# Performance work log

Measured on AMD Instinct MI355X. Metric: run time of the kernel, lower is better.

Reference implementation:

```python
import jax, jax.numpy as jnp
import numpy as np

T, B, I, H, NL = 512, 64, 1024, 1024, 2  # time, batch, input, hidden, layers


def setup_inputs() -> dict:
    key = jax.random.key(0)
    k0, k1, k2, k3, k4 = jax.random.split(key, 5)
    # xavier-uniform bound for W: [fan_in, 3*H]
    bound = float(np.sqrt(6.0 / (I + 3 * H)))
    x = jax.random.normal(k0, (T, B, I), jnp.float32)
    h0 = jax.random.normal(k1, (NL, B, H), jnp.float32) * 0.1  # initial hidden states
    W1 = jax.random.uniform(k2, (I, 3 * H), jnp.float32, -bound, bound)
    b1 = jnp.zeros((3 * H,), jnp.float32)
    W2 = jax.random.uniform(k3, (H, 3 * H), jnp.float32, -bound, bound)
    b2 = jnp.zeros((3 * H,), jnp.float32)
    L = jax.random.randint(k4, (B,), 0, T)  # per-example valid lengths
    return {"x": x, "h0": h0, "W1": W1, "b1": b1, "W2": W2, "b2": b2, "L": L}


def _lrn_layer(xs, h_init, W, b, L):
    # Hoist the input projection out of the time loop: same math as per-step mm.
    gates = jnp.einsum('tbi,ig->tbg', xs, W) + b          # [T, B, 3H]
    p, q, r = jnp.split(gates, 3, axis=-1)                 # each [T, B, H]
    # mask[t, b] = 1 if t < L[b] else 0 (keeps old state past sequence end)
    mask = (jnp.arange(xs.shape[0])[:, None] < L[None, :]).astype(xs.dtype)[:, :, None]

    def step(h, inp):
        pt, qt, rt, mt = inp
        i = jax.nn.sigmoid(pt + h)
        f = jax.nn.sigmoid(qt - h)
        nh = jnp.tanh(i * rt + f * h)
        nh = nh * mt + h * (1.0 - mt)
        return nh, nh

    h_last, out = jax.lax.scan(step, h_init, (p, q, r, mask))
    return out, h_last


def reference(x, h0, W1, b1, W2, b2, L):
    out1, h1 = _lrn_layer(x, h0[0], W1, b1, L)
    out2, h2 = _lrn_layer(out1, h0[1], W2, b2, L)   # dropout=0 -> identity between layers
    return out2, jnp.stack([h1, h2], axis=0)
```

## Files before the change

### kernel.cpp

```cpp
#include <hip/hip_runtime.h>

#define T_DIM 512
#define B_DIM 64
#define I_DIM 1024
#define H_DIM 1024
#define G3    3072
#define M_DIM (T_DIM * B_DIM)
#define K_DIM 1024
#define KT    16

typedef unsigned short u16;
typedef __bf16 bf16x8 __attribute__((ext_vector_type(8)));
typedef float  f32x4  __attribute__((ext_vector_type(4)));
typedef unsigned short u16x8 __attribute__((ext_vector_type(8)));

__device__ __forceinline__ u16 f2bf(float x) {
  union { float f; unsigned u; } v; v.f = x;
  unsigned r = v.u + 0x7fffu + ((v.u >> 16) & 1u);
  return (u16)(r >> 16);
}
__device__ __forceinline__ float bf2f(u16 x) {
  union { unsigned u; float f; } v; v.u = ((unsigned)x) << 16;
  return v.f;
}

__global__ void build_offsets_kernel(const int* __restrict__ L, int* __restrict__ meta) {
  __shared__ int cnt[T_DIM];
  __shared__ int Ls[B_DIM];
  const int t = threadIdx.x;
  if (t < B_DIM) Ls[t] = L[t];
  __syncthreads();
  int n = 0;
  #pragma unroll 8
  for (int b = 0; b < B_DIM; ++b) n += (Ls[b] > t) ? 1 : 0;
  cnt[t] = n;
  __syncthreads();
  if (t == 0) {
    int acc = 0;
    for (int s = 0; s < T_DIM; ++s) { int c = cnt[s]; cnt[s] = acc; acc += c; }
    meta[T_DIM] = acc;
    meta[513] = acc;
    meta[514] = (acc + 511) & ~511;
  }
  __syncthreads();
  meta[t] = cnt[t];
}

__global__ void build_crow_kernel(const int* __restrict__ L, const int* __restrict__ meta,
                                  int* __restrict__ crow) {
  const int t = blockIdx.x;
  const int b = threadIdx.x;
  const bool valid = t < L[b];
  unsigned long long mask = __ballot(valid);
  const int rank = __popcll(mask & ((1ull << b) - 1ull));
  if (valid) crow[(t << 6) + b] = meta[t] + rank;
}

__global__ void cast_gather_kernel(const float* __restrict__ in, const int* __restrict__ L,
                                   const int* __restrict__ crow, u16* __restrict__ out, int n8) {
  int idx = blockIdx.x * blockDim.x + threadIdx.x;
  int stride = gridDim.x * blockDim.x;
  for (int i = idx; i < n8; i += stride) {
    const int row = i >> 7;
    const int ch  = i & 127;
    const int b = row & 63, t = row >> 6;
    if (t >= L[b]) continue;
    const int cr = crow[row];
    const float4* p = (const float4*)(in + (size_t)row * 1024 + ch * 8);
    float4 a = p[0], bb = p[1];
    u16x8 o;
    o[0] = f2bf(a.x);  o[1] = f2bf(a.y);  o[2] = f2bf(a.z);  o[3] = f2bf(a.w);
    o[4] = f2bf(bb.x); o[5] = f2bf(bb.y); o[6] = f2bf(bb.z); o[7] = f2bf(bb.w);
    *(u16x8*)(out + (size_t)cr * 1024 + ch * 8) = o;
  }
}

__global__ void transpose_cast_kernel(const float* __restrict__ W,
                                      u16* __restrict__ Wt, int K, int N) {
  __shared__ float tile[32][33];
  int n0 = blockIdx.x * 32, k0 = blockIdx.y * 32;
  int tx = threadIdx.x, ty = threadIdx.y;
  #pragma unroll
  for (int dy = 0; dy < 32; dy += 8)
    tile[ty + dy][tx] = W[(size_t)(k0 + ty + dy) * N + n0 + tx];
  __syncthreads();
  #pragma unroll
  for (int dy = 0; dy < 32; dy += 8)
    Wt[(size_t)(n0 + ty + dy) * K + k0 + tx] = f2bf(tile[tx][ty + dy]);
}

__device__ __forceinline__ void gload_lds16(const void* g, void* l) {
  __builtin_amdgcn_global_load_lds(
      (const __attribute__((address_space(1))) void*)g,
      (__attribute__((address_space(3))) void*)l, 16, 0, 0);
}

__device__ __forceinline__ void stage_half(const u16* __restrict__ G, u16* lbuf,
                                           int rb, int k0, int w, int l) {
  const int cs   = (l & 7) ^ (l >> 3);
  const int rsub = l >> 3;
  #pragma unroll
  for (int r = 0; r < 2; ++r) {
    const int row0 = rb + r * 64 + w * 8;
    gload_lds16(G + (size_t)(row0 + rsub) * K_DIM + k0 + cs * 8,
                lbuf + (size_t)row0 * 64);
  }
}

__device__ __forceinline__ bf16x8 ldfrag(const u16* buf, int row, int ks, int fr, int g4) {
  const int slot = ((ks << 2) + g4) ^ (fr & 7);
  return *(const bf16x8*)(buf + (size_t)row * 64 + slot * 8);
}

__device__ __forceinline__ void read_a(const u16* buf, bf16x8 (&dst)[4][2],
                                       int rbase, int fr, int g4) {
  #pragma unroll
  for (int m = 0; m < 4; ++m) {
    dst[m][0] = ldfrag(buf, rbase + m * 16 + fr, 0, fr, g4);
    dst[m][1] = ldfrag(buf, rbase + m * 16 + fr, 1, fr, g4);
  }
}
__device__ __forceinline__ void read_b(const u16* buf, bf16x8 (&dst)[2][2],
                                       int rbase, int fr, int g4) {
  #pragma unroll
  for (int n = 0; n < 2; ++n) {
    dst[n][0] = ldfrag(buf, rbase + n * 16 + fr, 0, fr, g4);
    dst[n][1] = ldfrag(buf, rbase + n * 16 + fr, 1, fr, g4);
  }
}

#define BARRIER()  do { __builtin_amdgcn_s_barrier(); __builtin_amdgcn_sched_barrier(0); } while (0)
#define LGKM0()    do { asm volatile("s_waitcnt lgkmcnt(0)" ::: "memory"); __builtin_amdgcn_sched_barrier(0); } while (0)

#define MFMA_Q(ACC, AV, BV)                                                            \
  do {                                                                                 \
    __builtin_amdgcn_s_setprio(1);                                                     \
    _Pragma("unroll")                                                                  \
    for (int m = 0; m < 4; ++m)                                                        \
      _Pragma("unroll")                                                                \
      for (int n = 0; n < 2; ++n) {                                                    \
        ACC = __builtin_amdgcn_mfma_f32_16x16x32_bf16(AV[m][0], BV[n][0], ACC, 0, 0, 0); \
        ACC = __builtin_amdgcn_mfma_f32_16x16x32_bf16(AV[m][1], BV[n][1], ACC, 0, 0, 0); \
      }                                                                                \
    __builtin_amdgcn_s_setprio(0);                                                     \
  } while (0)

__global__ __launch_bounds__(512, 2) void gemm256_kernel(
    const u16* __restrict__ A, const u16* __restrict__ Bt,
    const float* __restrict__ bias, u16* __restrict__ C, int N,
    const int* __restrict__ meta) {
  __shared__ u16 As[2][256 * 64];
  __shared__ u16 Bs[2][256 * 64];
  const int tid = threadIdx.x;
  const int l  = tid & 63, w = tid >> 6;
  const int wm = w >> 2,  wn = w & 3;
  const int fr = l & 15,  g4 = l >> 4;

  const int ny   = meta[514] >> 8;
  const int nact = gridDim.x * ny;
  const int q    = nact >> 3;
  const int lin  = blockIdx.y * gridDim.x + blockIdx.x;
  const int idx  = lin >> 3;
  if (idx >= q) return;
  const int swz = (lin & 7) * q + idx;
  const int bx = swz % gridDim.x, by = swz / gridDim.x;
  const int bm = by * 256, bn = bx * 256;

  const u16* Ab = A  + (size_t)bm * K_DIM;
  const u16* Bb = Bt + (size_t)bn * K_DIM;

  stage_half(Ab, As[0], 0,   0,  w, l);
  stage_half(Ab, As[0], 128, 0,  w, l);
  stage_half(Bb, Bs[0], 0,   0,  w, l);
  stage_half(Bb, Bs[0], 128, 0,  w, l);
  stage_half(Ab, As[1], 0,   64, w, l);
  stage_half(Ab, As[1], 128, 64, w, l);
  stage_half(Bb, Bs[1], 0,   64, w, l);

  f32x4 acc[8][4] = {};
  bf16x8 av0[4][2], av1[4][2], bv0[2][2], bv1[2][2];

  for (int T = 0; T < KT - 1; ++T) {
    const u16* Ac = As[T & 1];
    const u16* Bc = Bs[T & 1];
    u16* Bn1 = Bs[(T + 1) & 1];
    u16* An2 = As[T & 1];        u16* Bn2 = Bs[T & 1];
    const int k1 = (T + 1) * 64, k2 = (T + 2) * 64;
    const bool st2 = (T + 2) < KT;

    asm volatile("s_waitcnt vmcnt(6)" ::: "memory");
    BARRIER();

    read_a(Ac, av0, wm * 128, fr, g4);
    read_b(Bc, bv0, wn * 64, fr, g4);
    stage_half(Bb, Bn1, 128, k1, w, l);
    LGKM0();

    MFMA_Q(acc[m][n], av0, bv0);
    read_b(Bc, bv1, wn * 64 + 32, fr, g4);
    LGKM0();

    MFMA_Q(acc[m][n + 2], av0, bv1);
    read_a(Ac, av1, wm * 128 + 64, fr, g4);
    LGKM0();
    BARRIER();

    if (st2) {
      stage_half(Ab, An2, 0,   k2, w, l);
      stage_half(Ab, An2, 128, k2, w, l);
      stage_half(Bb, Bn2, 0,   k2, w, l);
    }

    MFMA_Q(acc[m + 4][n + 2], av1, bv1);
    MFMA_Q(acc[m + 4][n],     av1, bv0);
  }

  {
    const u16* Ac = As[(KT - 1) & 1];
    const u16* Bc = Bs[(KT - 1) & 1];
    asm volatile("s_waitcnt vmcnt(0)" ::: "memory");
    BARRIER();
    #pragma unroll
    for (int m = 0; m < 4; ++m) {
      av0[m][0] = ldfrag(Ac, wm * 128 + m * 16 + fr, 0, fr, g4);
      av0[m][1] = ldfrag(Ac, wm * 128 + m * 16 + fr, 1, fr, g4);
      av1[m][0] = ldfrag(Ac, wm * 128 + (m + 4) * 16 + fr, 0, fr, g4);
      av1[m][1] = ldfrag(Ac, wm * 128 + (m + 4) * 16 + fr, 1, fr, g4);
    }
    #pragma unroll
    for (int n = 0; n < 2; ++n) {
      bv0[n][0] = ldfrag(Bc, wn * 64 + n * 16 + fr, 0, fr, g4);
      bv0[n][1] = ldfrag(Bc, wn * 64 + n * 16 + fr, 1, fr, g4);
      bv1[n][0] = ldfrag(Bc, wn * 64 + (n + 2) * 16 + fr, 0, fr, g4);
      bv1[n][1] = ldfrag(Bc, wn * 64 + (n + 2) * 16 + fr, 1, fr, g4);
    }
    LGKM0();
    MFMA_Q(acc[m][n],         av0, bv0);
    MFMA_Q(acc[m][n + 2],     av0, bv1);
    MFMA_Q(acc[m + 4][n + 2], av1, bv1);
    MFMA_Q(acc[m + 4][n],     av1, bv0);
    BARRIER();
  }

  float bb[4];
  #pragma unroll
  for (int j = 0; j < 4; ++j) bb[j] = bias[bn + wn * 64 + j * 16 + fr];

  u16* eb = (w < 4) ? ((u16*)As + (size_t)w * 8192)
                    : ((u16*)Bs + (size_t)(w - 4) * 8192);
  #pragma unroll
  for (int i = 0; i < 8; ++i)
    #pragma unroll
    for (int j = 0; j < 4; ++j)
      #pragma unroll
      for (int v = 0; v < 4; ++v) {
        const int row = i * 16 + g4 * 4 + v;
        const int col = j * 16 + fr;
        eb[row * 64 + (col ^ ((row & 12) << 2))] = f2bf(acc[i][j][v] + bb[j]);
      }
  LGKM0();
  #pragma unroll
  for (int c = 0; c < 16; ++c) {
    const int lrow = c * 8 + (l >> 3);
    const int lcol = (l & 7) * 8;
    u16x8 d = *(const u16x8*)&eb[lrow * 64 + (lcol ^ ((lrow & 12) << 2))];
    *(u16x8*)&C[(size_t)(bm + wm * 128 + lrow) * N + (bn + wn * 64 + lcol)] = d;
  }
}

template <int OUT_BF16>
__global__ void scan_kernel(const u16* __restrict__ gates,
                            const float* __restrict__ h0,
                            const int* __restrict__ L,
                            const int* __restrict__ crow,
                            u16* __restrict__ out_bf,
                            float* __restrict__ out_f,
                            float* __restrict__ hlast) {
  const int e = blockIdx.x * blockDim.x + threadIdx.x;
  const int b = e >> 10;
  const int j = e & 1023;
  float h = h0[e];
  const int Lb = L[b];
  const size_t o0 = (size_t)b * H_DIM + j;
  int t = 0;
  #pragma unroll 8
  for (; t < Lb; ++t) {
    const int cr = crow[(t << 6) + b];
    const size_t gt = (size_t)cr * G3 + j;
    float p = bf2f(gates[gt]);
    float q = bf2f(gates[gt + H_DIM]);
    float r = bf2f(gates[gt + 2 * H_DIM]);
    float ii = 1.f / (1.f + __expf(-(p + h)));
    float ff = 1.f / (1.f + __expf(-(q - h)));
    float u  = ii * r + ff * h;
    float e2 = __expf(2.f * u);
    h = 1.f - 2.f / (e2 + 1.f);
    if (OUT_BF16) out_bf[(size_t)cr * H_DIM + j] = f2bf(h);
    else          out_f [o0 + (size_t)t * (B_DIM * H_DIM)] = h;
  }
  if (!OUT_BF16) {
    for (; t < T_DIM; ++t)
      out_f[o0 + (size_t)t * (B_DIM * H_DIM)] = h;
  }
  hlast[o0] = h;
}

extern "C" void kernel_launch(void* const* d_in, const int* in_sizes, int n_in,
                              void* d_out, int out_size, void* d_ws, size_t ws_size,
                              hipStream_t stream) {
  const float* x  = (const float*)d_in[0];
  const float* h0 = (const float*)d_in[1];
  const float* W1 = (const float*)d_in[2];
  const float* b1 = (const float*)d_in[3];
  const float* W2 = (const float*)d_in[4];
  const float* b2 = (const float*)d_in[5];
  const int*   L  = (const int*)d_in[6];

  float* out2 = (float*)d_out;
  float* hl   = out2 + (size_t)T_DIM * B_DIM * H_DIM;

  char* w = (char*)d_ws;
  u16* xb    = (u16*)(w);
  u16* W1t   = (u16*)(w + (size_t)67108864);
  u16* W2t   = (u16*)(w + (size_t)73400320);
  u16* gates = (u16*)(w + (size_t)79691776);
  u16* out1  = (u16*)(w + (size_t)281018368);
  int* meta  = (int*)(w + (size_t)348127232);
  int* crow  = (int*)(w + (size_t)348131328);

  build_offsets_kernel<<<1, 512, 0, stream>>>(L, meta);
  build_crow_kernel<<<T_DIM, 64, 0, stream>>>(L, meta, crow);
  cast_gather_kernel<<<2048, 256, 0, stream>>>(x, L, crow, xb, (T_DIM * B_DIM * I_DIM) / 8);
  dim3 tb(32, 8);
  transpose_cast_kernel<<<dim3(G3 / 32, I_DIM / 32), tb, 0, stream>>>(W1, W1t, I_DIM, G3);
  transpose_cast_kernel<<<dim3(G3 / 32, H_DIM / 32), tb, 0, stream>>>(W2, W2t, H_DIM, G3);

  gemm256_kernel<<<dim3(G3 / 256, M_DIM / 256), 512, 0, stream>>>(
      xb, W1t, b1, gates, G3, meta);
  scan_kernel<1><<<(B_DIM * H_DIM) / 256, 256, 0, stream>>>(
      gates, h0, L, crow, out1, nullptr, hl);

  gemm256_kernel<<<dim3(G3 / 256, M_DIM / 256), 512, 0, stream>>>(
      out1, W2t, b2, gates, G3, meta);
  scan_kernel<0><<<(B_DIM * H_DIM) / 256, 256, 0, stream>>>(
      gates, h0 + B_DIM * H_DIM, L, crow, nullptr, out2, hl + B_DIM * H_DIM);
}
```

Baseline: 449.6 us.

## Software-pipeline scan gate loads with transposed row index and separate tail broadcast

The scan kernel now reads a per-batch transposed compacted-row table as int4 chunks and double-buffers gate loads four timesteps ahead, so global load latency overlaps the serial recurrence. The fill of padded timesteps past each sequence end moves out of the scan into a separate bandwidth-oriented broadcast kernel that copies the final hidden state, so the long serial scan threads no longer do it. The two weight transpose launches are merged into one grid with a z dimension. This adds a crowT table, more registers per scan thread and one extra launch.

```diff
diff --git a/kernel.cpp b/kernel.cpp
--- a/kernel.cpp
+++ b/kernel.cpp
@@ -47,13 +47,17 @@
 }
 
 __global__ void build_crow_kernel(const int* __restrict__ L, const int* __restrict__ meta,
-                                  int* __restrict__ crow) {
+                                  int* __restrict__ crow, int* __restrict__ crowT) {
   const int t = blockIdx.x;
   const int b = threadIdx.x;
   const bool valid = t < L[b];
   unsigned long long mask = __ballot(valid);
   const int rank = __popcll(mask & ((1ull << b) - 1ull));
-  if (valid) crow[(t << 6) + b] = meta[t] + rank;
+  if (valid) {
+    const int cr = meta[t] + rank;
+    crow[(t << 6) + b] = cr;
+    crowT[(b << 9) + t] = cr;
+  }
 }
 
 __global__ void cast_gather_kernel(const float* __restrict__ in, const int* __restrict__ L,
@@ -75,18 +79,20 @@
   }
 }
 
-__global__ void transpose_cast_kernel(const float* __restrict__ W,
-                                      u16* __restrict__ Wt, int K, int N) {
+__global__ void transpose_cast_kernel(const float* __restrict__ W1, const float* __restrict__ W2,
+                                      u16* __restrict__ W1t, u16* __restrict__ W2t) {
   __shared__ float tile[32][33];
+  const float* W = blockIdx.z ? W2 : W1;
+  u16* Wt       = blockIdx.z ? W2t : W1t;
   int n0 = blockIdx.x * 32, k0 = blockIdx.y * 32;
   int tx = threadIdx.x, ty = threadIdx.y;
   #pragma unroll
   for (int dy = 0; dy < 32; dy += 8)
-    tile[ty + dy][tx] = W[(size_t)(k0 + ty + dy) * N + n0 + tx];
+    tile[ty + dy][tx] = W[(size_t)(k0 + ty + dy) * G3 + n0 + tx];
   __syncthreads();
   #pragma unroll
   for (int dy = 0; dy < 32; dy += 8)
-    Wt[(size_t)(n0 + ty + dy) * K + k0 + tx] = f2bf(tile[tx][ty + dy]);
+    Wt[(size_t)(n0 + ty + dy) * K_DIM + k0 + tx] = f2bf(tile[tx][ty + dy]);
 }
 
 __device__ __forceinline__ void gload_lds16(const void* g, void* l) {
@@ -268,11 +274,41 @@
   }
 }
 
+__device__ __forceinline__ float stepf(float h, u16 gp, u16 gq, u16 gr) {
+  float p = bf2f(gp), q = bf2f(gq), r = bf2f(gr);
+  float ii = 1.f / (1.f + __expf(-(p + h)));
+  float ff = 1.f / (1.f + __expf(-(q - h)));
+  float u  = ii * r + ff * h;
+  float e2 = __expf(2.f * u);
+  return 1.f - 2.f / (e2 + 1.f);
+}
+
+#define LOADCHUNK(GP, GQ, GR, CR, cidx)                                        \
+  do {                                                                         \
+    int4 c4_ = crowT4[(b << 7) + (cidx)];                                      \
+    CR[0] = c4_.x; CR[1] = c4_.y; CR[2] = c4_.z; CR[3] = c4_.w;                \
+    _Pragma("unroll")                                                          \
+    for (int i_ = 0; i_ < 4; ++i_) {                                           \
+      const u16* g_ = gates + (size_t)CR[i_] * G3 + j;                         \
+      GP[i_] = g_[0]; GQ[i_] = g_[H_DIM]; GR[i_] = g_[2 * H_DIM];              \
+    }                                                                          \
+  } while (0)
+
+#define COMPUTE4(GP, GQ, GR, CR, cidx)                                         \
+  do {                                                                         \
+    _Pragma("unroll")                                                          \
+    for (int i_ = 0; i_ < 4; ++i_) {                                           \
+      h = stepf(h, GP[i_], GQ[i_], GR[i_]);                                    \
+      if (OUT_BF16) out_bf[(size_t)CR[i_] * H_DIM + j] = f2bf(h);              \
+      else out_f[o0 + (size_t)((cidx) * 4 + i_) * (B_DIM * H_DIM)] = h;        \
+    }                                                                          \
+  } while (0)
+
 template <int OUT_BF16>
 __global__ void scan_kernel(const u16* __restrict__ gates,
                             const float* __restrict__ h0,
                             const int* __restrict__ L,
-                            const int* __restrict__ crow,
+                            const int* __restrict__ crowT,
                             u16* __restrict__ out_bf,
                             float* __restrict__ out_f,
                             float* __restrict__ hlast) {
@@ -282,27 +318,45 @@
   float h = h0[e];
   const int Lb = L[b];
   const size_t o0 = (size_t)b * H_DIM + j;
-  int t = 0;
-  #pragma unroll 8
-  for (; t < Lb; ++t) {
-    const int cr = crow[(t << 6) + b];
-    const size_t gt = (size_t)cr * G3 + j;
-    float p = bf2f(gates[gt]);
-    float q = bf2f(gates[gt + H_DIM]);
-    float r = bf2f(gates[gt + 2 * H_DIM]);
-    float ii = 1.f / (1.f + __expf(-(p + h)));
-    float ff = 1.f / (1.f + __expf(-(q - h)));
-    float u  = ii * r + ff * h;
-    float e2 = __expf(2.f * u);
-    h = 1.f - 2.f / (e2 + 1.f);
+  const int4* crowT4 = (const int4*)crowT;
+
+  const int nfull = Lb >> 2;
+  int crA[4], crB[4];
+  u16 gpA[4], gqA[4], grA[4], gpB[4], gqB[4], grB[4];
+
+  if (nfull > 0) LOADCHUNK(gpA, gqA, grA, crA, 0);
+  int cc = 0;
+  #pragma unroll 1
+  while (cc < nfull) {
+    if (cc + 1 < nfull) LOADCHUNK(gpB, gqB, grB, crB, cc + 1);
+    COMPUTE4(gpA, gqA, grA, crA, cc);
+    ++cc;
+    if (cc < nfull) {
+      if (cc + 1 < nfull) LOADCHUNK(gpA, gqA, grA, crA, cc + 1);
+      COMPUTE4(gpB, gqB, grB, crB, cc);
+      ++cc;
+    }
+  }
+  for (int t = nfull * 4; t < Lb; ++t) {
+    const int cr = crowT[(b << 9) + t];
+    const u16* g = gates + (size_t)cr * G3 + j;
+    h = stepf(h, g[0], g[H_DIM], g[2 * H_DIM]);
     if (OUT_BF16) out_bf[(size_t)cr * H_DIM + j] = f2bf(h);
-    else          out_f [o0 + (size_t)t * (B_DIM * H_DIM)] = h;
-  }
-  if (!OUT_BF16) {
-    for (; t < T_DIM; ++t)
-      out_f[o0 + (size_t)t * (B_DIM * H_DIM)] = h;
+    else          out_f[o0 + (size_t)t * (B_DIM * H_DIM)] = h;
   }
   hlast[o0] = h;
+}
+
+__global__ void tail_bcast_kernel(const float* __restrict__ hlast2,
+                                  const int* __restrict__ L,
+                                  float* __restrict__ out2) {
+  for (int r = blockIdx.x; r < M_DIM; r += gridDim.x) {
+    const int t = r >> 6, b = r & 63;
+    if (t < L[b]) continue;
+    const float4* src = (const float4*)(hlast2 + (size_t)b * H_DIM);
+    float4* dst = (float4*)(out2 + (size_t)r * H_DIM);
+    dst[threadIdx.x] = src[threadIdx.x];
+  }
 }
 
 extern "C" void kernel_launch(void* const* d_in, const int* in_sizes, int n_in,
@@ -327,21 +381,22 @@
   u16* out1  = (u16*)(w + (size_t)281018368);
   int* meta  = (int*)(w + (size_t)348127232);
   int* crow  = (int*)(w + (size_t)348131328);
+  int* crowT = (int*)(w + (size_t)348262400);
 
   build_offsets_kernel<<<1, 512, 0, stream>>>(L, meta);
-  build_crow_kernel<<<T_DIM, 64, 0, stream>>>(L, meta, crow);
+  build_crow_kernel<<<T_DIM, 64, 0, stream>>>(L, meta, crow, crowT);
   cast_gather_kernel<<<2048, 256, 0, stream>>>(x, L, crow, xb, (T_DIM * B_DIM * I_DIM) / 8);
-  dim3 tb(32, 8);
-  transpose_cast_kernel<<<dim3(G3 / 32, I_DIM / 32), tb, 0, stream>>>(W1, W1t, I_DIM, G3);
-  transpose_cast_kernel<<<dim3(G3 / 32, H_DIM / 32), tb, 0, stream>>>(W2, W2t, H_DIM, G3);
+  transpose_cast_kernel<<<dim3(G3 / 32, K_DIM / 32, 2), dim3(32, 8), 0, stream>>>(
+      W1, W2, W1t, W2t);
 
   gemm256_kernel<<<dim3(G3 / 256, M_DIM / 256), 512, 0, stream>>>(
       xb, W1t, b1, gates, G3, meta);
   scan_kernel<1><<<(B_DIM * H_DIM) / 256, 256, 0, stream>>>(
-      gates, h0, L, crow, out1, nullptr, hl);
+      gates, h0, L, crowT, out1, nullptr, hl);
 
   gemm256_kernel<<<dim3(G3 / 256, M_DIM / 256), 512, 0, stream>>>(
       out1, W2t, b2, gates, G3, meta);
   scan_kernel<0><<<(B_DIM * H_DIM) / 256, 256, 0, stream>>>(
-      gates, h0 + B_DIM * H_DIM, L, crow, nullptr, out2, hl + B_DIM * H_DIM);
-}
+      gates, h0 + B_DIM * H_DIM, L, crowT, nullptr, out2, hl + B_DIM * H_DIM);
+  tail_bcast_kernel<<<2048, 256, 0, stream>>>(hl + B_DIM * H_DIM, L, out2);
+}
```

Result: slower. 588.4 us (+30.9%).
